# Kernel tuning notes

Hardware: AMD Instinct MI355X
Metric: run time of the kernel (lower is better)

The kernel has to match this reference:

```python
import jax, jax.numpy as jnp
import numpy as np

N = 50000
E = 800000

def sage_conv(x, src, dst, Wl, Wr, b):
    # PyG SAGEConv (mean aggr): out = lin_l(mean_{j in N(i)} x_j) + lin_r(x_i)
    ones = jnp.ones((src.shape[0],), x.dtype)
    deg = jax.ops.segment_sum(ones, dst, num_segments=N)          # [N]
    agg = jax.ops.segment_sum(x[src], dst, num_segments=N)        # [N, d]
    agg = agg / jnp.maximum(deg, 1.0)[:, None]                    # mean, 0 for isolated nodes
    return agg @ Wl + x @ Wr + b


def setup_inputs() -> dict:
    key = jax.random.key(0)
    ks = jax.random.split(key, 12)
    d_in, d_hid, d_mid, d_out = 128, 128, 256, 64
    sc = lambda d: 1.0 / np.sqrt(d)
    inp = {
        "x0": jax.random.normal(ks[0], (N, d_in), jnp.float32),
        "x1": jax.random.normal(ks[1], (N, d_in), jnp.float32),
        "edge_index": jax.random.randint(ks[2], (2, E), 0, N, dtype=jnp.int64),
        "Wl0": jax.random.normal(ks[3], (d_in, d_hid), jnp.float32) * sc(d_in),
        "Wr0": jax.random.normal(ks[4], (d_in, d_hid), jnp.float32) * sc(d_in),
        "b0": jnp.zeros((d_hid,), jnp.float32),
        "Wl1": jax.random.normal(ks[5], (d_in, d_hid), jnp.float32) * sc(d_in),
        "Wr1": jax.random.normal(ks[6], (d_in, d_hid), jnp.float32) * sc(d_in),
        "b1": jnp.zeros((d_hid,), jnp.float32),
        "Wlm": jax.random.normal(ks[7], (d_mid, d_mid), jnp.float32) * sc(d_mid),
        "Wrm": jax.random.normal(ks[8], (d_mid, d_mid), jnp.float32) * sc(d_mid),
        "bm": jnp.zeros((d_mid,), jnp.float32),
        "Wlo": jax.random.normal(ks[9], (d_mid, d_out), jnp.float32) * sc(d_mid),
        "Wro": jax.random.normal(ks[10], (d_mid, d_out), jnp.float32) * sc(d_mid),
        "bo": jnp.zeros((d_out,), jnp.float32),
    }
    return inp


def reference(x0, x1, edge_index, Wl0, Wr0, b0, Wl1, Wr1, b1, Wlm, Wrm, bm, Wlo, Wro, bo):
    src, dst = edge_index[0], edge_index[1]
    # initial branch convs + relu (dropout is identity in eval mode)
    h0 = jax.nn.relu(sage_conv(x0, src, dst, Wl0, Wr0, b0))
    h1 = jax.nn.relu(sage_conv(x1, src, dst, Wl1, Wr1, b1))
    h = jnp.concatenate([h0, h1], axis=-1)                        # [N, 256]
    # middle conv(s)
    h = jax.nn.relu(sage_conv(h, src, dst, Wlm, Wrm, bm))
    # final conv, no activation
    return sage_conv(h, src, dst, Wlo, Wro, bo)                   # [N, 64]
```

## Files before the change

### kernel.cpp

```cpp
#include <hip/hip_runtime.h>
#include <cstdint>
#include <cstddef>


typedef __attribute__((ext_vector_type(8))) short short8;
typedef __attribute__((ext_vector_type(4))) float f32x4;
typedef __attribute__((ext_vector_type(2))) float f32x2;

#define CAPLOG 6
#define CAP 64
#define BSH 7
#define MAXBUK 512
#define BCAP 2560
#define EPB 4096

__device__ __forceinline__ ushort f2bf(float f) {
    unsigned u = __float_as_uint(f);
    u += 0x7fffu + ((u >> 16) & 1u);
    return (ushort)(u >> 16);
}
__device__ __forceinline__ float bf2f(ushort u) {
    return __uint_as_float((unsigned)u << 16);
}
__device__ __forceinline__ void acc2(unsigned dw, f32x2& a) {
    f32x2 v;
    v.x = __uint_as_float(dw << 16);
    v.y = __uint_as_float(dw & 0xffff0000u);
    a += v;
}

__global__ void prep_kernel(
    int eb, int xb, int E, int N, int nbuk,
    const int* __restrict__ src, const int* __restrict__ dst,
    int* __restrict__ gcursor, unsigned* __restrict__ binned,
    const float* x0, const float* x1, ushort* xc,
    const float* __restrict__ Wl0, const float* __restrict__ Wr0,
    const float* __restrict__ Wl1, const float* __restrict__ Wr1,
    const float* __restrict__ Wlm, const float* __restrict__ Wrm,
    const float* __restrict__ Wlo, const float* __restrict__ Wro,
    const float* __restrict__ b0, const float* __restrict__ b1,
    ushort* __restrict__ Wcat1, ushort* __restrict__ Wcat2,
    ushort* __restrict__ Wcat3, float* __restrict__ bcat01) {
    __shared__ int hist[MAXBUK];
    int tid = threadIdx.x;
    if (blockIdx.x < eb) {
        for (int b = tid; b < MAXBUK; b += 256) hist[b] = 0;
        __syncthreads();
        int base = blockIdx.x * EPB;
        unsigned ep[16];
        unsigned rk[16];
#pragma unroll
        for (int j = 0; j < 16; ++j) {
            int i = base + j * 256 + tid;
            rk[j] = 0xFFFFFFFFu;
            if (i < E) {
                int s = src[i], d = dst[i];
                int b = d >> BSH;
                int r = atomicAdd(&hist[b], 1);
                ep[j] = ((unsigned)(d & ((1 << BSH) - 1)) << 16) | (unsigned)s;
                rk[j] = ((unsigned)b << 16) | (unsigned)r;
            }
        }
        __syncthreads();
        for (int b = tid; b < nbuk; b += 256) {
            int c = hist[b];
            hist[b] = c ? atomicAdd(&gcursor[b], c) : 0;
        }
        __syncthreads();
#pragma unroll
        for (int j = 0; j < 16; ++j) {
            if (rk[j] == 0xFFFFFFFFu) continue;
            int b = rk[j] >> 16;
            int pos = hist[b] + (int)(rk[j] & 0xFFFFu);
            if (pos < BCAP) binned[(size_t)b * BCAP + pos] = ep[j];
        }
        return;
    }
    if (blockIdx.x < eb + xb) {
        int gid = (blockIdx.x - eb) * blockDim.x + tid;
        int w = gid >> 5, lane = gid & 31;
        if (w >= N) return;
        float4 a = *((const float4*)(x0 + (size_t)w * 128) + lane);
        float4 b = *((const float4*)(x1 + (size_t)w * 128) + lane);
        ushort4 ua; ua.x = f2bf(a.x); ua.y = f2bf(a.y);
        ua.z = f2bf(a.z); ua.w = f2bf(a.w);
        ushort4 ub; ub.x = f2bf(b.x); ub.y = f2bf(b.y);
        ub.z = f2bf(b.z); ub.w = f2bf(b.w);
        *((ushort4*)(xc + (size_t)w * 256) + lane) = ua;
        *((ushort4*)(xc + (size_t)w * 256 + 128) + lane) = ub;
        return;
    }
    int idx = (blockIdx.x - eb - xb) * blockDim.x + tid;
    if (idx < 65536) {
        int n = idx >> 8, k = idx & 255;
        int half = n >> 7, nl = n & 127;
        const float* Wl = half ? Wl1 : Wl0;
        const float* Wr = half ? Wr1 : Wr0;
        float v = (k < 128) ? Wl[(size_t)k * 128 + nl]
                            : Wr[(size_t)(k - 128) * 128 + nl];
        Wcat1[idx] = f2bf(v);
    } else if (idx < 65536 + 131072) {
        int i2 = idx - 65536;
        int n = i2 >> 9, k = i2 & 511;
        float v = (k < 256) ? Wlm[(size_t)k * 256 + n]
                            : Wrm[(size_t)(k - 256) * 256 + n];
        Wcat2[i2] = f2bf(v);
    } else if (idx < 65536 + 131072 + 32768) {
        int i3 = idx - (65536 + 131072);
        int n = i3 >> 8, k = i3 & 255;
        float v = (n < 64) ? Wlo[(size_t)k * 64 + n]
                           : Wro[(size_t)k * 64 + (n - 64)];
        Wcat3[i3] = f2bf(v);
    } else if (idx < 65536 + 131072 + 32768 + 256) {
        int i4 = idx - (65536 + 131072 + 32768);
        bcat01[i4] = (i4 < 128) ? b0[i4] : b1[i4 - 128];
    }
}

__global__ void bin2col_kernel(const unsigned* __restrict__ binned,
                               const int* __restrict__ gcursor,
                               ushort* __restrict__ col,
                               int* __restrict__ deg, int N) {
    __shared__ int h2[1 << BSH];
    int tid = threadIdx.x;
    int b = blockIdx.x;
    if (tid < (1 << BSH)) h2[tid] = 0;
    __syncthreads();
    int cnt = min(gcursor[b], BCAP);
    for (int i = tid; i < cnt; i += 256) {
        unsigned e = binned[(size_t)b * BCAP + i];
        int ld = e >> 16;
        int r = atomicAdd(&h2[ld], 1);
        if (r < CAP)
            col[(((size_t)((b << BSH) + ld)) << CAPLOG) + r] = (ushort)(e & 0xFFFFu);
    }
    __syncthreads();
    if (tid < (1 << BSH)) {
        int d = (b << BSH) + tid;
        if (d < N) deg[d] = h2[tid];
    }
}

__device__ __forceinline__ int wave_sort64(int v, int lane) {
#pragma unroll
    for (int k = 2; k <= 64; k <<= 1) {
#pragma unroll
        for (int j = k >> 1; j > 0; j >>= 1) {
            int other = __shfl_xor(v, j, 64);
            bool takeMax = (((lane & j) != 0) == ((lane & k) == 0));
            v = takeMax ? max(v, other) : min(v, other);
        }
    }
    return v;
}


template <int SORT>
__global__ void agg_bf16_kernel(const ushort* __restrict__ src,
                                const int* __restrict__ deg,
                                ushort* __restrict__ col,
                                ushort* __restrict__ outt, int N) {
    int gid = blockIdx.x * blockDim.x + threadIdx.x;
    int w = gid >> 6, lane = gid & 63;
    if (w >= N) return;
    int len = min(deg[w], CAP);
    int beg = w << CAPLOG;
    int colv = (lane < len) ? (int)col[beg + lane] : 0x7fffffff;
    if (SORT) {
        colv = wave_sort64(colv, lane);
        if (lane < len) col[beg + lane] = (ushort)colv;
    }
    int hi = lane >> 5;
    int l16 = lane & 31;
    f32x2 s0 = {0.f, 0.f}, s1 = {0.f, 0.f}, s2 = {0.f, 0.f}, s3 = {0.f, 0.f};
    int pairs = len >> 1;
    int p = 0;
    for (; p + 8 <= pairs; p += 8) {
        uint4 v[8];
#pragma unroll
        for (int j = 0; j < 8; ++j) {
            int r0 = __builtin_amdgcn_readlane(colv, 2 * (p + j));
            int r1 = __builtin_amdgcn_readlane(colv, 2 * (p + j) + 1);
            int r = hi ? r1 : r0;
            v[j] = *((const uint4*)(src + (size_t)r * 256) + l16);
        }
#pragma unroll
        for (int j = 0; j < 8; ++j) {
            acc2(v[j].x, s0); acc2(v[j].y, s1);
            acc2(v[j].z, s2); acc2(v[j].w, s3);
        }
    }
    if (p + 4 <= pairs) {
        uint4 v[4];
#pragma unroll
        for (int j = 0; j < 4; ++j) {
            int r0 = __builtin_amdgcn_readlane(colv, 2 * (p + j));
            int r1 = __builtin_amdgcn_readlane(colv, 2 * (p + j) + 1);
            int r = hi ? r1 : r0;
            v[j] = *((const uint4*)(src + (size_t)r * 256) + l16);
        }
#pragma unroll
        for (int j = 0; j < 4; ++j) {
            acc2(v[j].x, s0); acc2(v[j].y, s1);
            acc2(v[j].z, s2); acc2(v[j].w, s3);
        }
        p += 4;
    }
    for (; p < pairs; ++p) {
        int r0 = __builtin_amdgcn_readlane(colv, 2 * p);
        int r1 = __builtin_amdgcn_readlane(colv, 2 * p + 1);
        int r = hi ? r1 : r0;
        uint4 v = *((const uint4*)(src + (size_t)r * 256) + l16);
        acc2(v.x, s0); acc2(v.y, s1); acc2(v.z, s2); acc2(v.w, s3);
    }
    if (len & 1) {
        int r = __builtin_amdgcn_readlane(colv, len - 1);
        if (lane < 32) {
            uint4 v = *((const uint4*)(src + (size_t)r * 256) + l16);
            acc2(v.x, s0); acc2(v.y, s1); acc2(v.z, s2); acc2(v.w, s3);
        }
    }
    s0.x += __shfl_xor(s0.x, 32, 64); s0.y += __shfl_xor(s0.y, 32, 64);
    s1.x += __shfl_xor(s1.x, 32, 64); s1.y += __shfl_xor(s1.y, 32, 64);
    s2.x += __shfl_xor(s2.x, 32, 64); s2.y += __shfl_xor(s2.y, 32, 64);
    s3.x += __shfl_xor(s3.x, 32, 64); s3.y += __shfl_xor(s3.y, 32, 64);
    if (lane < 32) {
        float inv = 1.0f / (float)max(len, 1);
        short8 o;
        o[0] = (short)f2bf(s0.x * inv); o[1] = (short)f2bf(s0.y * inv);
        o[2] = (short)f2bf(s1.x * inv); o[3] = (short)f2bf(s1.y * inv);
        o[4] = (short)f2bf(s2.x * inv); o[5] = (short)f2bf(s2.y * inv);
        o[6] = (short)f2bf(s3.x * inv); o[7] = (short)f2bf(s3.y * inv);
        *((short8*)(outt + (size_t)w * 256) + l16) = o;
    }
}


__global__ void agg64_add_kernel(const ushort* __restrict__ Z,
                                 const int* __restrict__ deg,
                                 const ushort* __restrict__ col,
                                 float* __restrict__ out, int N) {
    int gid = blockIdx.x * blockDim.x + threadIdx.x;
    int w = gid >> 6, lane = gid & 63;
    if (w >= N) return;
    int len = min(deg[w], CAP);
    int beg = w << CAPLOG;
    int colv = (lane < len) ? (int)col[beg + lane] : 0;
    int g = lane >> 4;
    int cl = lane & 15;
    f32x2 s0 = {0.f, 0.f}, s1 = {0.f, 0.f};
    int quads = len >> 2;
    int q = 0;
    for (; q + 4 <= quads; q += 4) {
        uint2 v[4];
#pragma unroll
        for (int j = 0; j < 4; ++j) {
            int qq = q + j;
            int r0 = __builtin_amdgcn_readlane(colv, 4 * qq);
            int r1 = __builtin_amdgcn_readlane(colv, 4 * qq + 1);
            int r2 = __builtin_amdgcn_readlane(colv, 4 * qq + 2);
            int r3 = __builtin_amdgcn_readlane(colv, 4 * qq + 3);
            int r01 = (g & 1) ? r1 : r0;
            int r23 = (g & 1) ? r3 : r2;
            int r = (g & 2) ? r23 : r01;
            v[j] = *((const uint2*)(Z + (size_t)r * 64) + cl);
        }
#pragma unroll
        for (int j = 0; j < 4; ++j) { acc2(v[j].x, s0); acc2(v[j].y, s1); }
    }
    for (; q < quads; ++q) {
        int r0 = __builtin_amdgcn_readlane(colv, 4 * q);
        int r1 = __builtin_amdgcn_readlane(colv, 4 * q + 1);
        int r2 = __builtin_amdgcn_readlane(colv, 4 * q + 2);
        int r3 = __builtin_amdgcn_readlane(colv, 4 * q + 3);
        int r01 = (g & 1) ? r1 : r0;
        int r23 = (g & 1) ? r3 : r2;
        int r = (g & 2) ? r23 : r01;
        uint2 v = *((const uint2*)(Z + (size_t)r * 64) + cl);
        acc2(v.x, s0); acc2(v.y, s1);
    }
    int rem = len & 3;
    if (rem) {
        int base = quads * 4;
        int i1 = min(base + 1, len - 1), i2 = min(base + 2, len - 1);
        int r0 = __builtin_amdgcn_readlane(colv, base);
        int r1 = __builtin_amdgcn_readlane(colv, i1);
        int r2 = __builtin_amdgcn_readlane(colv, i2);
        int r01 = (g & 1) ? r1 : r0;
        int r = (g & 2) ? r2 : r01;
        if (g < rem) {
            uint2 v = *((const uint2*)(Z + (size_t)r * 64) + cl);
            acc2(v.x, s0); acc2(v.y, s1);
        }
    }
    float f0 = s0.x, f1 = s0.y, f2 = s1.x, f3 = s1.y;
    f0 += __shfl_xor(f0, 16, 64); f0 += __shfl_xor(f0, 32, 64);
    f1 += __shfl_xor(f1, 16, 64); f1 += __shfl_xor(f1, 32, 64);
    f2 += __shfl_xor(f2, 16, 64); f2 += __shfl_xor(f2, 32, 64);
    f3 += __shfl_xor(f3, 16, 64); f3 += __shfl_xor(f3, 32, 64);
    if (lane < 16) {
        float inv = 1.0f / (float)max(len, 1);
        float4* po = (float4*)(out + (size_t)w * 64) + cl;
        float4 cur = *po;
        cur.x += f0 * inv; cur.y += f1 * inv;
        cur.z += f2 * inv; cur.w += f3 * inv;
        *po = cur;
    }
}

template <int K1, int K2, int MODE>
__global__ __launch_bounds__(256) void rs2_gemm_kernel(
    const ushort* __restrict__ A1, const ushort* __restrict__ A2, int lda,
    const ushort* __restrict__ Wg, const float* __restrict__ bias,
    ushort* __restrict__ D, float* __restrict__ D2, int M) {
    constexpr int KTOT = K1 + K2;
    constexpr int NCHUNK = KTOT / 128;
    constexpr int PK = 136;
    __shared__ __align__(16) ushort Bs[128 * PK];

    int y = blockIdx.y;
    if (MODE == 0) { A1 += y * 128; A2 += y * 128; }
    if (MODE != 2) {
        Wg += (size_t)y * 128 * KTOT;
        bias += y * 128;
        D += y * 128;
    }

    int tid = threadIdx.x;
    int m0 = blockIdx.x * 128;
    int wave = tid >> 6, lane = tid & 63;
    int lr = lane & 15, lq = lane >> 4;

    int mrow[2];
#pragma unroll
    for (int mt = 0; mt < 2; ++mt)
        mrow[mt] = min(m0 + wave * 32 + mt * 16 + lr, M - 1);

    f32x4 acc[2][8];
#pragma unroll
    for (int i = 0; i < 2; ++i)
#pragma unroll
        for (int j = 0; j < 8; ++j) acc[i][j] = (f32x4){0.f, 0.f, 0.f, 0.f};

    auto loadA = [&](int kp, short8* a) {
#pragma unroll
        for (int mt = 0; mt < 2; ++mt) {
            const ushort* srcp = (K2 == 0 || kp < K1)
                                     ? (A1 + (size_t)mrow[mt] * lda + kp)
                                     : (A2 + (size_t)mrow[mt] * lda + (kp - K1));
            a[mt] = *(const short8*)(srcp + lq * 8);
        }
    };

    short8 acur[2], anx[2];
    loadA(0, acur);

#pragma unroll
    for (int kc = 0; kc < NCHUNK; ++kc) {
        if (kc) __syncthreads();
#pragma unroll
        for (int i = 0; i < 8; ++i) {
            int e = (tid + i * 256) * 8;
            int row = e >> 7, colc = e & 127;
            float4 v = *(const float4*)(Wg + (size_t)row * KTOT + kc * 128 + colc);
            *(float4*)&Bs[row * PK + colc] = v;
        }
        __syncthreads();

#pragma unroll
        for (int ks = 0; ks < 4; ++ks) {
            int kpn = kc * 128 + (ks + 1) * 32;
            if (kpn < KTOT) loadA(kpn, anx);
            short8 b[8];
#pragma unroll
            for (int nt = 0; nt < 8; ++nt)
                b[nt] = *(const short8*)&Bs[(nt * 16 + lr) * PK + ks * 32 + lq * 8];
#pragma unroll
            for (int nt = 0; nt < 8; ++nt) {
                acc[0][nt] = __builtin_amdgcn_mfma_f32_16x16x32_bf16(
                    acur[0], b[nt], acc[0][nt], 0, 0, 0);
                acc[1][nt] = __builtin_amdgcn_mfma_f32_16x16x32_bf16(
                    acur[1], b[nt], acc[1][nt], 0, 0, 0);
            }
            acur[0] = anx[0];
            acur[1] = anx[1];
        }
    }

#pragma unroll
    for (int nt = 0; nt < 8; ++nt) {
        int c = nt * 16 + lr;
#pragma unroll
        for (int mt = 0; mt < 2; ++mt) {
#pragma unroll
            for (int r = 0; r < 4; ++r) {
                int m = m0 + wave * 32 + mt * 16 + lq * 4 + r;
                if (m >= M) continue;
                float v = acc[mt][nt][r];
                if (MODE == 2) {
                    if (c < 64) D[(size_t)m * 64 + c] = f2bf(v);
                    else        D2[(size_t)m * 64 + (c - 64)] = v + bias[c - 64];
                } else {
                    v = fmaxf(v + bias[c], 0.f);
                    D[(size_t)m * 256 + c] = f2bf(v);
                }
            }
        }
    }
}


extern "C" void kernel_launch(void* const* d_in, const int* in_sizes, int n_in,
                              void* d_out, int out_size, void* d_ws, size_t ws_size,
                              hipStream_t stream) {
    const float* x0 = (const float*)d_in[0];
    const float* x1 = (const float*)d_in[1];
    const int* ei = (const int*)d_in[2];
    const float* Wl0 = (const float*)d_in[3];
    const float* Wr0 = (const float*)d_in[4];
    const float* b0 = (const float*)d_in[5];
    const float* Wl1 = (const float*)d_in[6];
    const float* Wr1 = (const float*)d_in[7];
    const float* b1 = (const float*)d_in[8];
    const float* Wlm = (const float*)d_in[9];
    const float* Wrm = (const float*)d_in[10];
    const float* bm = (const float*)d_in[11];
    const float* Wlo = (const float*)d_in[12];
    const float* Wro = (const float*)d_in[13];
    const float* bo = (const float*)d_in[14];

    const int N = in_sizes[0] / 128;
    const int E = in_sizes[2] / 2;
    const int* srcI = ei;
    const int* dstI = ei + E;

    ushort* xc  = (ushort*)d_in[0];
    ushort* hb  = (ushort*)d_in[1];
    ushort* hmb = (ushort*)d_in[0];
    float* out = (float*)d_out;

    const int nbuk = (N + (1 << BSH) - 1) >> BSH;

    char* ws = (char*)d_ws;
    size_t used = 0;
    auto carve = [&](size_t bytes) {
        char* p = ws + used;
        used += (bytes + 63) & ~(size_t)63;
        return p;
    };
    int* deg = (int*)carve((size_t)N * 4);
    ushort* col = (ushort*)carve((size_t)N * CAP * 2);
    ushort* aggb = (ushort*)carve((size_t)N * 256 * 2);
    ushort* Zb   = (ushort*)carve((size_t)N * 64 * 2);
    unsigned* binned = (unsigned*)carve((size_t)nbuk * BCAP * 4);
    int* gcursor = (int*)carve((size_t)nbuk * 4);
    ushort* Wcat1 = (ushort*)carve(256 * 256 * 2);
    ushort* Wcat2 = (ushort*)carve(256 * 512 * 2);
    ushort* Wcat3 = (ushort*)carve(128 * 256 * 2);
    float* bcat01 = (float*)carve(256 * 4);
    if (used > ws_size) return;

    const int eb = (E + EPB - 1) / EPB;
    const int xb = (N * 32 + 255) / 256;
    const int ab = (N * 64 + 255) / 256;
    const int wb = (229632 + 255) / 256;
    const int gb = (N + 127) / 128;
    const ushort* UN = nullptr;

    hipMemsetAsync(gcursor, 0, (size_t)nbuk * 4, stream);
    prep_kernel<<<eb + xb + wb, 256, 0, stream>>>(
        eb, xb, E, N, nbuk, srcI, dstI, gcursor, binned, x0, x1, xc,
        Wl0, Wr0, Wl1, Wr1, Wlm, Wrm, Wlo, Wro, b0, b1,
        Wcat1, Wcat2, Wcat3, bcat01);
    bin2col_kernel<<<nbuk, 256, 0, stream>>>(binned, gcursor, col, deg, N);

    agg_bf16_kernel<1><<<ab, 256, 0, stream>>>(xc, deg, col, aggb, N);
    rs2_gemm_kernel<128, 128, 0><<<dim3(gb, 2), 256, 0, stream>>>(
        aggb, xc, 256, Wcat1, bcat01, hb, nullptr, N);

    agg_bf16_kernel<0><<<ab, 256, 0, stream>>>(hb, deg, col, aggb, N);
    rs2_gemm_kernel<256, 256, 1><<<dim3(gb, 2), 256, 0, stream>>>(
        aggb, hb, 256, Wcat2, bm, hmb, nullptr, N);

    rs2_gemm_kernel<256, 0, 2><<<dim3(gb, 1), 256, 0, stream>>>(
        hmb, UN, 256, Wcat3, bo, Zb, out, N);
    agg64_add_kernel<<<ab, 256, 0, stream>>>(Zb, deg, col, out, N);
}
```

Before: 365.2 us.

## Split gather-aggregation into column bands across interleaved blocks for cache locality

The aggregation kernels now split each node's feature row into 32-column bands, one per block, with consecutive block IDs covering the bands of the same four nodes. Each wave gathers four neighbors at a time with 4-byte loads instead of wide row loads. The wave-level bitonic sort of neighbor indices is dropped, so the neighbor order stays unsorted. The intent is that each band's working set fits better in cache and that more blocks run in parallel, at the cost of narrower loads, more blocks, and the index and degree loads repeated for every band.

```diff
diff --git a/kernel.cpp b/kernel.cpp
--- a/kernel.cpp
+++ b/kernel.cpp
@@ -18,9 +18,6 @@
     unsigned u = __float_as_uint(f);
     u += 0x7fffu + ((u >> 16) & 1u);
     return (ushort)(u >> 16);
-}
-__device__ __forceinline__ float bf2f(ushort u) {
-    return __uint_as_float((unsigned)u << 16);
 }
 __device__ __forceinline__ void acc2(unsigned dw, f32x2& a) {
     f32x2 v;
@@ -141,118 +138,26 @@
     }
 }
 
-__device__ __forceinline__ int wave_sort64(int v, int lane) {
-#pragma unroll
-    for (int k = 2; k <= 64; k <<= 1) {
-#pragma unroll
-        for (int j = k >> 1; j > 0; j >>= 1) {
-            int other = __shfl_xor(v, j, 64);
-            bool takeMax = (((lane & j) != 0) == ((lane & k) == 0));
-            v = takeMax ? max(v, other) : min(v, other);
-        }
-    }
-    return v;
-}
-
-
-template <int SORT>
+
 __global__ void agg_bf16_kernel(const ushort* __restrict__ src,
                                 const int* __restrict__ deg,
-                                ushort* __restrict__ col,
+                                const ushort* __restrict__ col,
                                 ushort* __restrict__ outt, int N) {
-    int gid = blockIdx.x * blockDim.x + threadIdx.x;
-    int w = gid >> 6, lane = gid & 63;
-    if (w >= N) return;
-    int len = min(deg[w], CAP);
-    int beg = w << CAPLOG;
-    int colv = (lane < len) ? (int)col[beg + lane] : 0x7fffffff;
-    if (SORT) {
-        colv = wave_sort64(colv, lane);
-        if (lane < len) col[beg + lane] = (ushort)colv;
-    }
-    int hi = lane >> 5;
-    int l16 = lane & 31;
-    f32x2 s0 = {0.f, 0.f}, s1 = {0.f, 0.f}, s2 = {0.f, 0.f}, s3 = {0.f, 0.f};
-    int pairs = len >> 1;
-    int p = 0;
-    for (; p + 8 <= pairs; p += 8) {
-        uint4 v[8];
-#pragma unroll
-        for (int j = 0; j < 8; ++j) {
-            int r0 = __builtin_amdgcn_readlane(colv, 2 * (p + j));
-            int r1 = __builtin_amdgcn_readlane(colv, 2 * (p + j) + 1);
-            int r = hi ? r1 : r0;
-            v[j] = *((const uint4*)(src + (size_t)r * 256) + l16);
-        }
-#pragma unroll
-        for (int j = 0; j < 8; ++j) {
-            acc2(v[j].x, s0); acc2(v[j].y, s1);
-            acc2(v[j].z, s2); acc2(v[j].w, s3);
-        }
-    }
-    if (p + 4 <= pairs) {
-        uint4 v[4];
-#pragma unroll
-        for (int j = 0; j < 4; ++j) {
-            int r0 = __builtin_amdgcn_readlane(colv, 2 * (p + j));
-            int r1 = __builtin_amdgcn_readlane(colv, 2 * (p + j) + 1);
-            int r = hi ? r1 : r0;
-            v[j] = *((const uint4*)(src + (size_t)r * 256) + l16);
-        }
-#pragma unroll
-        for (int j = 0; j < 4; ++j) {
-            acc2(v[j].x, s0); acc2(v[j].y, s1);
-            acc2(v[j].z, s2); acc2(v[j].w, s3);
-        }
-        p += 4;
-    }
-    for (; p < pairs; ++p) {
-        int r0 = __builtin_amdgcn_readlane(colv, 2 * p);
-        int r1 = __builtin_amdgcn_readlane(colv, 2 * p + 1);
-        int r = hi ? r1 : r0;
-        uint4 v = *((const uint4*)(src + (size_t)r * 256) + l16);
-        acc2(v.x, s0); acc2(v.y, s1); acc2(v.z, s2); acc2(v.w, s3);
-    }
-    if (len & 1) {
-        int r = __builtin_amdgcn_readlane(colv, len - 1);
-        if (lane < 32) {
-            uint4 v = *((const uint4*)(src + (size_t)r * 256) + l16);
-            acc2(v.x, s0); acc2(v.y, s1); acc2(v.z, s2); acc2(v.w, s3);
-        }
-    }
-    s0.x += __shfl_xor(s0.x, 32, 64); s0.y += __shfl_xor(s0.y, 32, 64);
-    s1.x += __shfl_xor(s1.x, 32, 64); s1.y += __shfl_xor(s1.y, 32, 64);
-    s2.x += __shfl_xor(s2.x, 32, 64); s2.y += __shfl_xor(s2.y, 32, 64);
-    s3.x += __shfl_xor(s3.x, 32, 64); s3.y += __shfl_xor(s3.y, 32, 64);
-    if (lane < 32) {
-        float inv = 1.0f / (float)max(len, 1);
-        short8 o;
-        o[0] = (short)f2bf(s0.x * inv); o[1] = (short)f2bf(s0.y * inv);
-        o[2] = (short)f2bf(s1.x * inv); o[3] = (short)f2bf(s1.y * inv);
-        o[4] = (short)f2bf(s2.x * inv); o[5] = (short)f2bf(s2.y * inv);
-        o[6] = (short)f2bf(s3.x * inv); o[7] = (short)f2bf(s3.y * inv);
-        *((short8*)(outt + (size_t)w * 256) + l16) = o;
-    }
-}
-
-
-__global__ void agg64_add_kernel(const ushort* __restrict__ Z,
-                                 const int* __restrict__ deg,
-                                 const ushort* __restrict__ col,
-                                 float* __restrict__ out, int N) {
-    int gid = blockIdx.x * blockDim.x + threadIdx.x;
-    int w = gid >> 6, lane = gid & 63;
+    int bid = blockIdx.x;
+    int s = bid & 7;
+    int wave = threadIdx.x >> 6, lane = threadIdx.x & 63;
+    int w = (bid >> 3) * 4 + wave;
     if (w >= N) return;
     int len = min(deg[w], CAP);
     int beg = w << CAPLOG;
     int colv = (lane < len) ? (int)col[beg + lane] : 0;
-    int g = lane >> 4;
-    int cl = lane & 15;
-    f32x2 s0 = {0.f, 0.f}, s1 = {0.f, 0.f};
+    int g = lane >> 4, cl = lane & 15;
+    const ushort* band = src + s * 32;
+    f32x2 acc = {0.f, 0.f};
     int quads = len >> 2;
     int q = 0;
     for (; q + 4 <= quads; q += 4) {
-        uint2 v[4];
+        unsigned v[4];
 #pragma unroll
         for (int j = 0; j < 4; ++j) {
             int qq = q + j;
@@ -263,10 +168,10 @@
             int r01 = (g & 1) ? r1 : r0;
             int r23 = (g & 1) ? r3 : r2;
             int r = (g & 2) ? r23 : r01;
-            v[j] = *((const uint2*)(Z + (size_t)r * 64) + cl);
-        }
-#pragma unroll
-        for (int j = 0; j < 4; ++j) { acc2(v[j].x, s0); acc2(v[j].y, s1); }
+            v[j] = *((const unsigned*)(band + (size_t)r * 256) + cl);
+        }
+#pragma unroll
+        for (int j = 0; j < 4; ++j) acc2(v[j], acc);
     }
     for (; q < quads; ++q) {
         int r0 = __builtin_amdgcn_readlane(colv, 4 * q);
@@ -276,8 +181,8 @@
         int r01 = (g & 1) ? r1 : r0;
         int r23 = (g & 1) ? r3 : r2;
         int r = (g & 2) ? r23 : r01;
-        uint2 v = *((const uint2*)(Z + (size_t)r * 64) + cl);
-        acc2(v.x, s0); acc2(v.y, s1);
+        unsigned v = *((const unsigned*)(band + (size_t)r * 256) + cl);
+        acc2(v, acc);
     }
     int rem = len & 3;
     if (rem) {
@@ -289,21 +194,90 @@
         int r01 = (g & 1) ? r1 : r0;
         int r = (g & 2) ? r2 : r01;
         if (g < rem) {
-            uint2 v = *((const uint2*)(Z + (size_t)r * 64) + cl);
-            acc2(v.x, s0); acc2(v.y, s1);
-        }
-    }
-    float f0 = s0.x, f1 = s0.y, f2 = s1.x, f3 = s1.y;
+            unsigned v = *((const unsigned*)(band + (size_t)r * 256) + cl);
+            acc2(v, acc);
+        }
+    }
+    float f0 = acc.x, f1 = acc.y;
     f0 += __shfl_xor(f0, 16, 64); f0 += __shfl_xor(f0, 32, 64);
     f1 += __shfl_xor(f1, 16, 64); f1 += __shfl_xor(f1, 32, 64);
-    f2 += __shfl_xor(f2, 16, 64); f2 += __shfl_xor(f2, 32, 64);
-    f3 += __shfl_xor(f3, 16, 64); f3 += __shfl_xor(f3, 32, 64);
     if (lane < 16) {
         float inv = 1.0f / (float)max(len, 1);
-        float4* po = (float4*)(out + (size_t)w * 64) + cl;
-        float4 cur = *po;
+        unsigned o = (unsigned)f2bf(f0 * inv) | ((unsigned)f2bf(f1 * inv) << 16);
+        *((unsigned*)(outt + (size_t)w * 256 + s * 32) + cl) = o;
+    }
+}
+
+
+__global__ void agg64_add_kernel(const ushort* __restrict__ Z,
+                                 const int* __restrict__ deg,
+                                 const ushort* __restrict__ col,
+                                 float* __restrict__ out, int N, int bpb) {
+    int bid = blockIdx.x;
+    int h = (bid & 7) >> 2;
+    int lb = (bid >> 3) * 4 + (bid & 3);
+    if (lb >= bpb) return;
+    int wave = threadIdx.x >> 6, lane = threadIdx.x & 63;
+    int w = lb * 4 + wave;
+    if (w >= N) return;
+    int len = min(deg[w], CAP);
+    int beg = w << CAPLOG;
+    int colv = (lane < len) ? (int)col[beg + lane] : 0;
+    int g = lane >> 4, cl = lane & 15;
+    const ushort* band = Z + h * 32;
+    f32x2 acc = {0.f, 0.f};
+    int quads = len >> 2;
+    int q = 0;
+    for (; q + 4 <= quads; q += 4) {
+        unsigned v[4];
+#pragma unroll
+        for (int j = 0; j < 4; ++j) {
+            int qq = q + j;
+            int r0 = __builtin_amdgcn_readlane(colv, 4 * qq);
+            int r1 = __builtin_amdgcn_readlane(colv, 4 * qq + 1);
+            int r2 = __builtin_amdgcn_readlane(colv, 4 * qq + 2);
+            int r3 = __builtin_amdgcn_readlane(colv, 4 * qq + 3);
+            int r01 = (g & 1) ? r1 : r0;
+            int r23 = (g & 1) ? r3 : r2;
+            int r = (g & 2) ? r23 : r01;
+            v[j] = *((const unsigned*)(band + (size_t)r * 64) + cl);
+        }
+#pragma unroll
+        for (int j = 0; j < 4; ++j) acc2(v[j], acc);
+    }
+    for (; q < quads; ++q) {
+        int r0 = __builtin_amdgcn_readlane(colv, 4 * q);
+        int r1 = __builtin_amdgcn_readlane(colv, 4 * q + 1);
+        int r2 = __builtin_amdgcn_readlane(colv, 4 * q + 2);
+        int r3 = __builtin_amdgcn_readlane(colv, 4 * q + 3);
+        int r01 = (g & 1) ? r1 : r0;
+        int r23 = (g & 1) ? r3 : r2;
+        int r = (g & 2) ? r23 : r01;
+        unsigned v = *((const unsigned*)(band + (size_t)r * 64) + cl);
+        acc2(v, acc);
+    }
+    int rem = len & 3;
+    if (rem) {
+        int base = quads * 4;
+        int i1 = min(base + 1, len - 1), i2 = min(base + 2, len - 1);
+        int r0 = __builtin_amdgcn_readlane(colv, base);
+        int r1 = __builtin_amdgcn_readlane(colv, i1);
+        int r2 = __builtin_amdgcn_readlane(colv, i2);
+        int r01 = (g & 1) ? r1 : r0;
+        int r = (g & 2) ? r2 : r01;
+        if (g < rem) {
+            unsigned v = *((const unsigned*)(band + (size_t)r * 64) + cl);
+            acc2(v, acc);
+        }
+    }
+    float f0 = acc.x, f1 = acc.y;
+    f0 += __shfl_xor(f0, 16, 64); f0 += __shfl_xor(f0, 32, 64);
+    f1 += __shfl_xor(f1, 16, 64); f1 += __shfl_xor(f1, 32, 64);
+    if (lane < 16) {
+        float inv = 1.0f / (float)max(len, 1);
+        float2* po = (float2*)(out + (size_t)w * 64 + h * 32) + cl;
+        float2 cur = *po;
         cur.x += f0 * inv; cur.y += f1 * inv;
-        cur.z += f2 * inv; cur.w += f3 * inv;
         *po = cur;
     }
 }
@@ -462,9 +436,10 @@
 
     const int eb = (E + EPB - 1) / EPB;
     const int xb = (N * 32 + 255) / 256;
-    const int ab = (N * 64 + 255) / 256;
     const int wb = (229632 + 255) / 256;
     const int gb = (N + 127) / 128;
+    const int bps = (N + 3) / 4;
+    const int g64 = ((bps + 3) / 4) * 8;
     const ushort* UN = nullptr;
 
     hipMemsetAsync(gcursor, 0, (size_t)nbuk * 4, stream);
@@ -474,15 +449,15 @@
         Wcat1, Wcat2, Wcat3, bcat01);
     bin2col_kernel<<<nbuk, 256, 0, stream>>>(binned, gcursor, col, deg, N);
 
-    agg_bf16_kernel<1><<<ab, 256, 0, stream>>>(xc, deg, col, aggb, N);
+    agg_bf16_kernel<<<bps * 8, 256, 0, stream>>>(xc, deg, col, aggb, N);
     rs2_gemm_kernel<128, 128, 0><<<dim3(gb, 2), 256, 0, stream>>>(
         aggb, xc, 256, Wcat1, bcat01, hb, nullptr, N);
 
-    agg_bf16_kernel<0><<<ab, 256, 0, stream>>>(hb, deg, col, aggb, N);
+    agg_bf16_kernel<<<bps * 8, 256, 0, stream>>>(hb, deg, col, aggb, N);
     rs2_gemm_kernel<256, 256, 1><<<dim3(gb, 2), 256, 0, stream>>>(
         aggb, hb, 256, Wcat2, bm, hmb, nullptr, N);
 
     rs2_gemm_kernel<256, 0, 2><<<dim3(gb, 1), 256, 0, stream>>>(
         hmb, UN, 256, Wcat3, bo, Zb, out, N);
-    agg64_add_kernel<<<ab, 256, 0, stream>>>(Zb, deg, col, out, N);
-}
+    agg64_add_kernel<<<g64, 256, 0, stream>>>(Zb, deg, col, out, N, bps);
+}
```

New measurement: 541.7 us. 48.3% more time.
